# Kernel tuning notes

Hardware: AMD Instinct MI355X
Metric: run time of the kernel (lower is better)

## Reference

```python
import jax, jax.numpy as jnp
import numpy as np

N, E, D_IN, H, OUT = 50000, 800000, 128, 256, 2
BN_EPS = 1e-5
LN_EPS = 1e-5


def _xavier(k, fi, fo):
    lim = float(np.sqrt(6.0 / (fi + fo)))
    return jax.random.uniform(k, (fi, fo), minval=-lim, maxval=lim, dtype=jnp.float32)


def setup_inputs() -> dict:
    key = jax.random.key(0)
    ks = jax.random.split(key, 8)
    return {
        "x": jax.random.normal(ks[0], (N, D_IN), dtype=jnp.float32),
        "edge_index": jax.random.randint(ks[1], (2, E), 0, N, dtype=jnp.int32),
        "feature_scale": jnp.ones((D_IN,), jnp.float32),
        "feature_bias": jnp.zeros((D_IN,), jnp.float32),
        "bn0_g": jnp.ones((D_IN,), jnp.float32),
        "bn0_b": jnp.zeros((D_IN,), jnp.float32),
        "W1": _xavier(ks[2], D_IN, H), "b1": jnp.zeros((H,), jnp.float32),
        "bn1_g": jnp.ones((H,), jnp.float32), "bn1_b": jnp.zeros((H,), jnp.float32),
        "ln1_g": jnp.ones((H,), jnp.float32), "ln1_b": jnp.zeros((H,), jnp.float32),
        "W2": _xavier(ks[3], H, H), "b2": jnp.zeros((H,), jnp.float32),
        "bn2_g": jnp.ones((H,), jnp.float32), "bn2_b": jnp.zeros((H,), jnp.float32),
        "ln2_g": jnp.ones((H,), jnp.float32), "ln2_b": jnp.zeros((H,), jnp.float32),
        "Wout": _xavier(ks[4], H, OUT), "bout": jnp.zeros((OUT,), jnp.float32),
    }


def _batchnorm(x, g, b):
    # training-mode BatchNorm1d: batch stats over node axis, biased variance
    mu = jnp.mean(x, axis=0)
    var = jnp.mean(jnp.square(x - mu), axis=0)
    return g * (x - mu) * jax.lax.rsqrt(var + BN_EPS) + b


def _layernorm(x, g, b):
    mu = jnp.mean(x, axis=-1, keepdims=True)
    var = jnp.mean(jnp.square(x - mu), axis=-1, keepdims=True)
    return g * (x - mu) * jax.lax.rsqrt(var + LN_EPS) + b


def _gcn(x, W, b, src, dst, dinv):
    # PyG GCNConv with self-loops: D^{-1/2}(A+I)D^{-1/2} X W + b
    h = x @ W                                   # [N, F]
    norm = (dinv[src] * dinv[dst])[:, None]     # [E, 1]
    msg = h[src] * norm                         # [E, F] (dominant traffic)
    agg = jax.ops.segment_sum(msg, dst, num_segments=N)
    return agg + (dinv * dinv)[:, None] * h + b


def _forward(x, feature_scale, feature_bias, bn0_g, bn0_b,
             W1, b1, bn1_g, bn1_b, ln1_g, ln1_b,
             W2, b2, bn2_g, bn2_b, ln2_g, ln2_b,
             Wout, bout, edge_index):
    src, dst = edge_index[0], edge_index[1]
    deg = jax.ops.segment_sum(jnp.ones((E,), x.dtype), dst, num_segments=N) + 1.0
    dinv = jax.lax.rsqrt(deg)

    h = x * feature_scale + feature_bias
    h = _batchnorm(h, bn0_g, bn0_b)            # input_bn; dropout = identity (eval)

    # layer 0 (no residual: i == 0)
    h1 = _gcn(h, W1, b1, src, dst, dinv)
    h1 = jax.nn.relu(h1)
    h1 = _batchnorm(h1, bn1_g, bn1_b)
    h1 = _layernorm(h1, ln1_g, ln1_b)

    # layer 1 (residual add, shapes match)
    h2 = _gcn(h1, W2, b2, src, dst, dinv)
    h2 = jax.nn.relu(h2)
    h2 = _batchnorm(h2, bn2_g, bn2_b)
    h2 = _layernorm(h2, ln2_g, ln2_b)
    h2 = h2 + h1

    return h2 @ Wout + bout


def reference(x, edge_index, feature_scale, feature_bias, bn0_g, bn0_b,
              W1, b1, bn1_g, bn1_b, ln1_g, ln1_b,
              W2, b2, bn2_g, bn2_b, ln2_g, ln2_b,
              Wout, bout):
    return _forward(x, feature_scale, feature_bias, bn0_g, bn0_b,
                    W1, b1, bn1_g, bn1_b, ln1_g, ln1_b,
                    W2, b2, bn2_g, bn2_b, ln2_g, ln2_b,
                    Wout, bout, edge_index)
```

## Files before the change

kernel.cpp:

```cpp
#include <hip/hip_runtime.h>
#include <hip/hip_bf16.h>
#include <stdint.h>

#define N_NODES 50000
#define N_EDGES 800000
#define D_IN    128
#define H_DIM   256
#define BN_EPS  1e-5f
#define LN_EPS  1e-5f
#define NBLK2 1563
#define SLICE_ELEMS ((size_t)N_NODES * 32)
#define EDGE_CHUNK 3072
#define BN0_BLOCKS 256
#define PREPX_BLOCKS 6250
#define TR_BLOCKS 256
#define NBKT 196
#define CHUNK 4096
#define RCHUNKS 196

typedef float v4f __attribute__((ext_vector_type(4)));
typedef short v8s __attribute__((ext_vector_type(8)));

__device__ __forceinline__ float bflo(unsigned u){ return __uint_as_float(u << 16); }
__device__ __forceinline__ float bfhi(unsigned u){ return __uint_as_float(u & 0xffff0000u); }
__device__ __forceinline__ unsigned short f2bf(float f){
  unsigned u = __float_as_uint(f);
  u += 0x7fffu + ((u >> 16) & 1u);
  return (unsigned short)(u >> 16);
}
__device__ __forceinline__ unsigned pack2(float a, float b){
  return (unsigned)f2bf(a) | ((unsigned)f2bf(b) << 16);
}
__device__ __forceinline__ float wred(float v){
  #pragma unroll
  for (int m = 1; m < 64; m <<= 1) v += __shfl_xor(v, m, 64);
  return v;
}

__device__ __forceinline__ int block_excl_scan(int v){
  int t = threadIdx.x;
  int lane = t & 63, w = t >> 6;
  int inc = v;
  #pragma unroll
  for (int m = 1; m < 64; m <<= 1){
    int o = __shfl_up(inc, m, 64);
    if (lane >= m) inc += o;
  }
  __shared__ int wsum[4];
  if (lane == 63) wsum[w] = inc;
  __syncthreads();
  int base = 0;
  #pragma unroll
  for (int j = 0; j < 4; ++j) if (j < w) base += wsum[j];
  return base + inc - v;
}

__global__ __launch_bounds__(256) void bn0r1_k(const int* ei, const float* x,
                                               const float* fs, const float* fb,
                                               float* S, float* Q, int* ghist){
  int b = blockIdx.x, t = threadIdx.x;
  if (b >= BN0_BLOCKS){
    __shared__ int lh[NBKT];
    int b2 = b - BN0_BLOCKS;
    for (int i = t; i < NBKT; i += 256) lh[i] = 0;
    __syncthreads();
    int e0 = b2 * CHUNK;
    int n = min(CHUNK, N_EDGES - e0);
    for (int i = t; i < n; i += 256)
      atomicAdd(&lh[ei[N_EDGES + e0 + i] >> 8], 1);
    __syncthreads();
    if (t < NBKT && lh[t] > 0) atomicAdd(&ghist[t], lh[t]);
    return;
  }
  int cl = t & 31, rg = t >> 5;
  int c = cl * 4;
  float4 fs4 = *(const float4*)(fs + c);
  float4 fb4 = *(const float4*)(fb + c);
  float s0=0,s1=0,s2=0,s3=0,q0=0,q1=0,q2=0,q3=0;
  for (int row = b * 8 + rg; row < N_NODES; row += BN0_BLOCKS * 8){
    float4 xv = *(const float4*)(x + (size_t)row * D_IN + c);
    float v0 = xv.x * fs4.x + fb4.x;
    float v1 = xv.y * fs4.y + fb4.y;
    float v2 = xv.z * fs4.z + fb4.z;
    float v3 = xv.w * fs4.w + fb4.w;
    s0 += v0; s1 += v1; s2 += v2; s3 += v3;
    q0 += v0*v0; q1 += v1*v1; q2 += v2*v2; q3 += v3*v3;
  }
  __shared__ float red[256][8];
  red[t][0]=s0; red[t][1]=s1; red[t][2]=s2; red[t][3]=s3;
  red[t][4]=q0; red[t][5]=q1; red[t][6]=q2; red[t][7]=q3;
  __syncthreads();
  float* Sr = S + (b & 3) * D_IN;
  float* Qr = Q + (b & 3) * D_IN;
  if (t < 32){
    float a[8];
    #pragma unroll
    for (int i = 0; i < 8; ++i) a[i] = red[t][i];
    for (int j = 1; j < 8; ++j)
      #pragma unroll
      for (int i = 0; i < 8; ++i) a[i] += red[t + 32*j][i];
    #pragma unroll
    for (int i = 0; i < 4; ++i){ atomicAdd(&Sr[t*4+i], a[i]); atomicAdd(&Qr[t*4+i], a[4+i]); }
  }
}

__global__ __launch_bounds__(256) void scanb_k(const int* ghist, int* gcursor, int* bbase){
  int t = threadIdx.x;
  int v = (t < NBKT) ? ghist[t] : 0;
  int e = block_excl_scan(v);
  if (t < NBKT){ gcursor[t] = e; bbase[t] = e; }
  if (t == 0) bbase[NBKT] = N_EDGES;
}

__global__ __launch_bounds__(256) void r3_k(const int* ei, int* gcursor, unsigned* ebuf){
  __shared__ unsigned short dstS[CHUNK];
  __shared__ int lh[NBKT], cb[NBKT];
  int t = threadIdx.x;
  int e0 = blockIdx.x * CHUNK;
  int n = min(CHUNK, N_EDGES - e0);
  for (int i = t; i < NBKT; i += 256) lh[i] = 0;
  __syncthreads();
  for (int i = t; i < n; i += 256){
    int d = ei[N_EDGES + e0 + i];
    dstS[i] = (unsigned short)d;
    atomicAdd(&lh[d >> 8], 1);
  }
  __syncthreads();
  if (t < NBKT && lh[t] > 0) cb[t] = atomicAdd(&gcursor[t], lh[t]);
  __syncthreads();
  if (t < NBKT) lh[t] = 0;
  __syncthreads();
  for (int i = t; i < n; i += 256){
    int d = dstS[i];
    int bkt = d >> 8;
    int r = atomicAdd(&lh[bkt], 1);
    unsigned src = (unsigned)ei[e0 + i];
    ebuf[cb[bkt] + r] = ((unsigned)(d & 255) << 16) | src;
  }
}

__global__ __launch_bounds__(256) void r4a_k(const unsigned* ebuf, const int* bbase,
                                             int* cnt, int* dhist){
  __shared__ int h[256], dh[128];
  int t = threadIdx.x, b = blockIdx.x;
  h[t] = 0;
  if (t < 128) dh[t] = 0;
  __syncthreads();
  int lo = bbase[b], hi = bbase[b + 1];
  for (int i = lo + t; i < hi; i += 256)
    atomicAdd(&h[(ebuf[i] >> 16) & 255], 1);
  __syncthreads();
  int node = b * 256 + t;
  if (node < N_NODES){
    cnt[node] = h[t];
    atomicAdd(&dh[min(h[t], 127)], 1);
  }
  __syncthreads();
  if (t < 128 && dh[t] > 0) atomicAdd(&dhist[t], dh[t]);
}

__global__ __launch_bounds__(256) void dperm2_k(const int* cnt, const int* dhist, int* reserve,
                                                int* perm, int* rank, int* offs, float* dinv){
  __shared__ int ep_s[128], W_s[128], lb[128], lh[128], lc[128];
  int t = threadIdx.x;
  int v = (t < 128) ? dhist[t] : 0;
  int e1 = block_excl_scan(v);
  __syncthreads();
  int e2 = block_excl_scan((t < 128) ? v * t : 0);
  __syncthreads();
  if (t < 128){ ep_s[t] = e1; W_s[t] = e2; lh[t] = 0; lc[t] = 0; }
  __syncthreads();
  for (int i = blockIdx.x * 256 + t; i < N_NODES; i += 32 * 256)
    atomicAdd(&lh[min(cnt[i], 127)], 1);
  __syncthreads();
  if (t < 128 && lh[t] > 0) lb[t] = ep_s[t] + atomicAdd(&reserve[t], lh[t]);
  __syncthreads();
  for (int i = blockIdx.x * 256 + t; i < N_NODES; i += 32 * 256){
    int d = cnt[i];
    int b = min(d, 127);
    int r = atomicAdd(&lc[b], 1);
    int pos = lb[b] + r;
    perm[pos] = i;
    rank[i] = pos;
    offs[pos] = W_s[b] + (pos - ep_s[b]) * d;
    dinv[i] = rsqrtf((float)d + 1.0f);
  }
  if (blockIdx.x == 0 && t == 0) offs[N_NODES] = N_EDGES;
}

__global__ __launch_bounds__(256) void r4b_k(const unsigned* ebuf, const int* bbase,
                                             const int* rank, const int* offs,
                                             unsigned short* edges){
  __shared__ int curs[256];
  int t = threadIdx.x, b = blockIdx.x;
  int node = b * 256 + t;
  if (node < N_NODES) curs[t] = offs[rank[node]];
  __syncthreads();
  int lo = bbase[b], hi = bbase[b + 1];
  for (int i = lo + t; i < hi; i += 256){
    unsigned u = ebuf[i];
    int l8 = (u >> 16) & 255;
    int pos = atomicAdd(&curs[l8], 1);
    edges[pos] = (unsigned short)(u & 0xffffu);
  }
}

__global__ __launch_bounds__(256) void prep_k(const float* x, const float* S, const float* Q,
                                              const float* fs, const float* fb,
                                              const float* gg, const float* bb,
                                              unsigned short* xt,
                                              const float* W1, const float* W2,
                                              unsigned short* W1t, unsigned short* W2t){
  int b = blockIdx.x, t = threadIdx.x;
  if (b < PREPX_BLOCKS){
    int i = b * 256 + t;
    int row = i >> 5; int c = (i & 31) * 4;
    float4 Sv = *(const float4*)(S + c);
    float4 Qv = *(const float4*)(Q + c);
    #pragma unroll
    for (int rep = 1; rep < 4; ++rep){
      float4 s2 = *(const float4*)(S + rep * D_IN + c);
      float4 q2 = *(const float4*)(Q + rep * D_IN + c);
      Sv.x += s2.x; Sv.y += s2.y; Sv.z += s2.z; Sv.w += s2.w;
      Qv.x += q2.x; Qv.y += q2.y; Qv.z += q2.z; Qv.w += q2.w;
    }
    float4 fs4 = *(const float4*)(fs + c);
    float4 fb4 = *(const float4*)(fb + c);
    float4 gg4 = *(const float4*)(gg + c);
    float4 bb4 = *(const float4*)(bb + c);
    const float invN = 1.0f / N_NODES;
    float mu0 = Sv.x*invN, mu1 = Sv.y*invN, mu2 = Sv.z*invN, mu3 = Sv.w*invN;
    float r0 = rsqrtf(Qv.x*invN - mu0*mu0 + BN_EPS);
    float r1 = rsqrtf(Qv.y*invN - mu1*mu1 + BN_EPS);
    float r2 = rsqrtf(Qv.z*invN - mu2*mu2 + BN_EPS);
    float r3 = rsqrtf(Qv.w*invN - mu3*mu3 + BN_EPS);
    float a0 = gg4.x*r0*fs4.x, c0 = gg4.x*r0*(fb4.x - mu0) + bb4.x;
    float a1 = gg4.y*r1*fs4.y, c1 = gg4.y*r1*(fb4.y - mu1) + bb4.y;
    float a2 = gg4.z*r2*fs4.z, c2 = gg4.z*r2*(fb4.z - mu2) + bb4.z;
    float a3 = gg4.w*r3*fs4.w, c3 = gg4.w*r3*(fb4.w - mu3) + bb4.w;
    float4 xv = *(const float4*)(x + (size_t)row * D_IN + c);
    uint2 o;
    o.x = pack2(a0 * xv.x + c0, a1 * xv.y + c1);
    o.y = pack2(a2 * xv.z + c2, a3 * xv.w + c3);
    *(uint2*)(xt + (size_t)row * D_IN + c) = o;
    return;
  }
  int i = (b - PREPX_BLOCKS) * 256 + t;
  if (i < D_IN * H_DIM){
    int r = i / H_DIM, c = i % H_DIM;
    W1t[c * D_IN + r] = f2bf(W1[i]);
  }
  if (i < H_DIM * H_DIM){
    int r = i / H_DIM, c = i % H_DIM;
    W2t[c * H_DIM + r] = f2bf(W2[i]);
  }
}

template<int K>
__global__ __launch_bounds__(256) void gemm_k(const unsigned short* A, const unsigned short* Bt,
                                              const float* dinv, unsigned short* C, int M){
  __shared__ __align__(16) short smem[16896];
  __shared__ float dvs[64];
  short* As = smem;
  short* Bs = smem + 64 * 40;
  int t = threadIdx.x;
  int m0 = blockIdx.x * 64;
  int lane = t & 63;
  int w = t >> 6;
  int fr = lane & 15, quad = lane >> 4;
  if (t < 64) dvs[t] = (m0 + t < M) ? dinv[m0 + t] : 0.0f;
  v4f acc[4][4] = {};
  int sr = t >> 2;
  int sk = (t & 3) << 3;
  for (int k0 = 0; k0 < K; k0 += 32){
    __syncthreads();
    uint4 av = {0,0,0,0};
    int arow = m0 + sr;
    if (arow < M) av = *(const uint4*)(A + (size_t)arow * K + k0 + sk);
    *(uint4*)(&As[sr * 40 + sk]) = av;
    #pragma unroll
    for (int j = 0; j < 4; ++j){
      int brow = sr + 64 * j;
      uint4 bv = *(const uint4*)(Bt + (size_t)brow * K + k0 + sk);
      *(uint4*)(&Bs[brow * 40 + sk]) = bv;
    }
    __syncthreads();
    v8s af[4], bf[4];
    #pragma unroll
    for (int mi = 0; mi < 4; ++mi)
      af[mi] = *(const v8s*)(&As[(mi * 16 + fr) * 40 + quad * 8]);
    #pragma unroll
    for (int ni = 0; ni < 4; ++ni)
      bf[ni] = *(const v8s*)(&Bs[(w * 64 + ni * 16 + fr) * 40 + quad * 8]);
    #pragma unroll
    for (int mi = 0; mi < 4; ++mi)
      #pragma unroll
      for (int ni = 0; ni < 4; ++ni)
        acc[mi][ni] = __builtin_amdgcn_mfma_f32_16x16x32_bf16(af[mi], bf[ni], acc[mi][ni], 0, 0, 0);
  }
  __syncthreads();
  short* Cs = smem;
  #pragma unroll
  for (int mi = 0; mi < 4; ++mi)
    #pragma unroll
    for (int ni = 0; ni < 4; ++ni)
      #pragma unroll
      for (int r = 0; r < 4; ++r){
        int row = mi * 16 + quad * 4 + r;
        int col = w * 64 + ni * 16 + fr;
        Cs[row * 264 + col] = (short)f2bf(acc[mi][ni][r] * dvs[row]);
      }
  __syncthreads();
  int orow = t >> 2;
  int grow = m0 + orow;
  if (grow < M){
    #pragma unroll
    for (int j = 0; j < 4; ++j){
      int oc = (t & 3) * 16 + 64 * j;
      v8s v0 = *(const v8s*)(&Cs[orow * 264 + oc]);
      v8s v1 = *(const v8s*)(&Cs[orow * 264 + oc + 8]);
      *(v8s*)(&C[(size_t)(oc >> 5) * SLICE_ELEMS + (size_t)grow * 32 + (oc & 31)]) = v0;
      int oc1 = oc + 8;
      *(v8s*)(&C[(size_t)(oc1 >> 5) * SLICE_ELEMS + (size_t)grow * 32 + (oc1 & 31)]) = v1;
    }
  }
}

__global__ __launch_bounds__(256) void agg_k(const unsigned short* hs, const int* offsets,
                                             const unsigned short* edges, const int* perm,
                                             const float* dinv, const float* bias,
                                             unsigned short* g, float* pS, float* pQ){
  __shared__ unsigned eds32[EDGE_CHUNK / 2];
  __shared__ float wps[4][8][8];
  int t = threadIdx.x;
  int lane = t & 63;
  int wv = t >> 6;
  int slice = blockIdx.x & 7;
  int l8 = lane & 7;
  int nb = (blockIdx.x >> 3) * 32;
  int idx = nb + (t >> 3);
  int lastn = min(nb + 32, N_NODES);
  int blk0 = offsets[nb];
  int base = blk0 & ~1;
  int blkN = offsets[lastn];
  const unsigned* gsrc = (const unsigned*)(edges + base);
  int nu = min((blkN - base + 1) >> 1, EDGE_CHUNK / 2);
  for (int i = t; i < nu; i += 256)
    eds32[i] = gsrc[i];
  __syncthreads();
  bool act = idx < N_NODES;
  int node = act ? perm[idx] : 0;
  const unsigned short* hb = hs + (size_t)slice * SLICE_ELEMS;
  float4 bb = *(const float4*)(bias + slice * 32 + l8 * 4);
  uint2 sv = *(const uint2*)(hb + (size_t)node * 32 + l8 * 4);
  float a0 = bflo(sv.x), a1 = bfhi(sv.x);
  float a2 = bflo(sv.y), a3 = bfhi(sv.y);
  int e  = act ? offsets[idx] : 0;
  int e1 = act ? offsets[idx + 1] : 0;
  if ((e & 1) && e < e1){
    int ru = (e - base) >> 1;
    unsigned d = (ru < EDGE_CHUNK / 2) ? eds32[ru] : gsrc[ru];
    unsigned s = d >> 16;
    uint2 v = *(const uint2*)(hb + (size_t)s * 32 + l8 * 4);
    a0 += bflo(v.x); a1 += bfhi(v.x);
    a2 += bflo(v.y); a3 += bfhi(v.y);
    ++e;
  }
  for (; e + 16 <= e1; e += 16){
    int ru = (e - base) >> 1;
    unsigned dd[8];
    if (ru + 8 <= EDGE_CHUNK / 2){
      #pragma unroll
      for (int j = 0; j < 8; ++j) dd[j] = eds32[ru + j];
    } else {
      #pragma unroll
      for (int j = 0; j < 8; ++j) dd[j] = gsrc[ru + j];
    }
    uint2 v[16];
    #pragma unroll
    for (int j = 0; j < 8; ++j){
      v[2*j]   = *(const uint2*)(hb + (size_t)(dd[j] & 0xffffu) * 32 + l8 * 4);
      v[2*j+1] = *(const uint2*)(hb + (size_t)(dd[j] >> 16)     * 32 + l8 * 4);
    }
    #pragma unroll
    for (int j = 0; j < 16; ++j){
      a0 += bflo(v[j].x); a1 += bfhi(v[j].x);
      a2 += bflo(v[j].y); a3 += bfhi(v[j].y);
    }
  }
  if (e + 8 <= e1){
    int ru = (e - base) >> 1;
    unsigned dd[4];
    if (ru + 4 <= EDGE_CHUNK / 2){
      #pragma unroll
      for (int j = 0; j < 4; ++j) dd[j] = eds32[ru + j];
    } else {
      #pragma unroll
      for (int j = 0; j < 4; ++j) dd[j] = gsrc[ru + j];
    }
    uint2 v[8];
    #pragma unroll
    for (int j = 0; j < 4; ++j){
      v[2*j]   = *(const uint2*)(hb + (size_t)(dd[j] & 0xffffu) * 32 + l8 * 4);
      v[2*j+1] = *(const uint2*)(hb + (size_t)(dd[j] >> 16)     * 32 + l8 * 4);
    }
    #pragma unroll
    for (int j = 0; j < 8; ++j){
      a0 += bflo(v[j].x); a1 += bfhi(v[j].x);
      a2 += bflo(v[j].y); a3 += bfhi(v[j].y);
    }
    e += 8;
  }
  for (; e < e1; ++e){
    int r = e - base;
    unsigned d = ((r >> 1) < EDGE_CHUNK / 2) ? eds32[r >> 1] : gsrc[r >> 1];
    unsigned s = (r & 1) ? (d >> 16) : (d & 0xffffu);
    uint2 v = *(const uint2*)(hb + (size_t)s * 32 + l8 * 4);
    a0 += bflo(v.x); a1 += bfhi(v.x);
    a2 += bflo(v.y); a3 += bfhi(v.y);
  }
  float dv = dinv[node];
  float y0 = act ? fmaxf(dv * a0 + bb.x, 0.f) : 0.f;
  float y1 = act ? fmaxf(dv * a1 + bb.y, 0.f) : 0.f;
  float y2 = act ? fmaxf(dv * a2 + bb.z, 0.f) : 0.f;
  float y3 = act ? fmaxf(dv * a3 + bb.w, 0.f) : 0.f;
  if (act){
    uint2 o;
    o.x = pack2(y0, y1); o.y = pack2(y2, y3);
    *(uint2*)(g + (size_t)node * H_DIM + slice * 32 + l8 * 4) = o;
  }
  float q0 = y0*y0, q1 = y1*y1, q2 = y2*y2, q3 = y3*y3;
  #pragma unroll
  for (int m = 8; m < 64; m <<= 1){
    y0 += __shfl_xor(y0, m, 64); y1 += __shfl_xor(y1, m, 64);
    y2 += __shfl_xor(y2, m, 64); y3 += __shfl_xor(y3, m, 64);
    q0 += __shfl_xor(q0, m, 64); q1 += __shfl_xor(q1, m, 64);
    q2 += __shfl_xor(q2, m, 64); q3 += __shfl_xor(q3, m, 64);
  }
  if (lane < 8){
    wps[wv][l8][0] = y0; wps[wv][l8][1] = y1; wps[wv][l8][2] = y2; wps[wv][l8][3] = y3;
    wps[wv][l8][4] = q0; wps[wv][l8][5] = q1; wps[wv][l8][6] = q2; wps[wv][l8][7] = q3;
  }
  __syncthreads();
  if (t < 64){
    int tl8 = t >> 3, ti = t & 7;
    float v = wps[0][tl8][ti] + wps[1][tl8][ti] + wps[2][tl8][ti] + wps[3][tl8][ti];
    int col32 = tl8 * 4 + (ti & 3);
    if (ti < 4) pS[(size_t)blockIdx.x * 32 + col32] = v;
    else        pQ[(size_t)blockIdx.x * 32 + col32] = v;
  }
}

__global__ __launch_bounds__(1024) void redu_k(const float* pS, const float* pQ,
                                               const float* gg, const float* bb,
                                               float* sc, float* sh){
  __shared__ float ls[32][32], lq[32][32];
  int t = threadIdx.x;
  int slice = blockIdx.x;
  int grp = t >> 5, c32 = t & 31;
  float as = 0.f, aq = 0.f;
  for (int blk2 = grp; blk2 < NBLK2; blk2 += 32){
    size_t o = ((size_t)blk2 * 8 + slice) * 32 + c32;
    as += pS[o]; aq += pQ[o];
  }
  ls[grp][c32] = as; lq[grp][c32] = aq;
  __syncthreads();
  if (t < 32){
    float S = 0.f, Q = 0.f;
    #pragma unroll
    for (int gI = 0; gI < 32; ++gI){ S += ls[gI][t]; Q += lq[gI][t]; }
    int col = slice * 32 + t;
    const float invN = 1.0f / N_NODES;
    float mu = S * invN;
    float rs = rsqrtf(Q * invN - mu * mu + BN_EPS);
    float s = gg[col] * rs;
    sc[col] = s;
    sh[col] = bb[col] - s * mu;
  }
}

__global__ __launch_bounds__(256) void apply1_k(const unsigned short* g, const float* sc, const float* sh,
                                                const float* lng, const float* lnb, unsigned short* h1){
  int lane = threadIdx.x & 63;
  int row = blockIdx.x * 4 + (threadIdx.x >> 6);
  if (row >= N_NODES) return;
  int c = lane * 4;
  float4 s4 = *(const float4*)(sc + c);
  float4 h4 = *(const float4*)(sh + c);
  uint2 u = *(const uint2*)(g + (size_t)row * H_DIM + c);
  float v0 = s4.x * bflo(u.x) + h4.x;
  float v1 = s4.y * bfhi(u.x) + h4.y;
  float v2 = s4.z * bflo(u.y) + h4.z;
  float v3 = s4.w * bfhi(u.y) + h4.w;
  float sum = wred(v0 + v1 + v2 + v3);
  float sq  = wred(v0*v0 + v1*v1 + v2*v2 + v3*v3);
  float mu = sum * (1.0f / H_DIM);
  float var = sq * (1.0f / H_DIM) - mu * mu;
  float rs = rsqrtf(var + LN_EPS);
  float4 g4 = *(const float4*)(lng + c);
  float4 b4 = *(const float4*)(lnb + c);
  float y0 = g4.x * (v0 - mu) * rs + b4.x;
  float y1 = g4.y * (v1 - mu) * rs + b4.y;
  float y2 = g4.z * (v2 - mu) * rs + b4.z;
  float y3 = g4.w * (v3 - mu) * rs + b4.w;
  uint2 o; o.x = pack2(y0, y1); o.y = pack2(y2, y3);
  *(uint2*)(h1 + (size_t)row * H_DIM + c) = o;
}

__global__ __launch_bounds__(256) void apply2_k(const unsigned short* g, const float* sc, const float* sh,
                                                const float* lng, const float* lnb,
                                                const unsigned short* h1, const float* Wout,
                                                const float* bout, float* out){
  int lane = threadIdx.x & 63;
  int row = blockIdx.x * 4 + (threadIdx.x >> 6);
  if (row >= N_NODES) return;
  int c = lane * 4;
  float4 s4 = *(const float4*)(sc + c);
  float4 h4 = *(const float4*)(sh + c);
  uint2 u = *(const uint2*)(g + (size_t)row * H_DIM + c);
  float v0 = s4.x * bflo(u.x) + h4.x;
  float v1 = s4.y * bfhi(u.x) + h4.y;
  float v2 = s4.z * bflo(u.y) + h4.z;
  float v3 = s4.w * bfhi(u.y) + h4.w;
  float sum = wred(v0 + v1 + v2 + v3);
  float sq  = wred(v0*v0 + v1*v1 + v2*v2 + v3*v3);
  float mu = sum * (1.0f / H_DIM);
  float var = sq * (1.0f / H_DIM) - mu * mu;
  float rs = rsqrtf(var + LN_EPS);
  float4 g4 = *(const float4*)(lng + c);
  float4 b4 = *(const float4*)(lnb + c);
  uint2 hr = *(const uint2*)(h1 + (size_t)row * H_DIM + c);
  float y0 = g4.x * (v0 - mu) * rs + b4.x + bflo(hr.x);
  float y1 = g4.y * (v1 - mu) * rs + b4.y + bfhi(hr.x);
  float y2 = g4.z * (v2 - mu) * rs + b4.z + bflo(hr.y);
  float y3 = g4.w * (v3 - mu) * rs + b4.w + bfhi(hr.y);
  float4 w0 = *(const float4*)(Wout + c * 2);
  float4 w1 = *(const float4*)(Wout + c * 2 + 4);
  float o0 = y0 * w0.x + y1 * w0.z + y2 * w1.x + y3 * w1.z;
  float o1 = y0 * w0.y + y1 * w0.w + y2 * w1.y + y3 * w1.w;
  o0 = wred(o0); o1 = wred(o1);
  if (lane == 0){
    out[(size_t)row * 2 + 0] = o0 + bout[0];
    out[(size_t)row * 2 + 1] = o1 + bout[1];
  }
}

extern "C" void kernel_launch(void* const* d_in, const int* in_sizes, int n_in,
                              void* d_out, int out_size, void* d_ws, size_t ws_size,
                              hipStream_t stream) {
  const float* x    = (const float*)d_in[0];
  const int*   ei   = (const int*)d_in[1];
  const float* fs   = (const float*)d_in[2];
  const float* fb   = (const float*)d_in[3];
  const float* bn0g = (const float*)d_in[4];
  const float* bn0b = (const float*)d_in[5];
  const float* W1   = (const float*)d_in[6];
  const float* b1   = (const float*)d_in[7];
  const float* bn1g = (const float*)d_in[8];
  const float* bn1b = (const float*)d_in[9];
  const float* ln1g = (const float*)d_in[10];
  const float* ln1b = (const float*)d_in[11];
  const float* W2   = (const float*)d_in[12];
  const float* b2   = (const float*)d_in[13];
  const float* bn2g = (const float*)d_in[14];
  const float* bn2b = (const float*)d_in[15];
  const float* ln2g = (const float*)d_in[16];
  const float* ln2b = (const float*)d_in[17];
  const float* Wout = (const float*)d_in[18];
  const float* bout = (const float*)d_in[19];
  float* out = (float*)d_out;

  char* w = (char*)d_ws;
  float* bn0S  = (float*)(w + 0);
  float* bn0Q  = (float*)(w + 2048);
  int*   dhist = (int*)(w + 4096);
  int*   reserve = (int*)(w + 4608);
  int*   ghist  = (int*)(w + 5120);
  int*   gcursor= (int*)(w + 5904);
  const size_t ZERO_BYTES = 6688;
  int*   bbase  = (int*)(w + 6688);
  float* sc1   = (float*)(w + 7488);
  float* sh1   = (float*)(w + 8512);
  float* sc2   = (float*)(w + 9536);
  float* sh2   = (float*)(w + 10560);
  int*   cnt   = (int*)(w + 11584);
  float* dinv  = (float*)(w + 211584);
  int*   offs  = (int*)(w + 411584);
  int*   perm  = (int*)(w + 611712);
  int*   rank  = (int*)(w + 811712);
  unsigned short* edges = (unsigned short*)(w + 1011712);
  unsigned short* xt   = (unsigned short*)(w + 2611712);
  unsigned short* W1t  = (unsigned short*)(w + 15411712);
  unsigned short* W2t  = (unsigned short*)(w + 15477248);
  unsigned short* hlin = (unsigned short*)(w + 15608320);
  unsigned*       ebuf = (unsigned*)(w + 15608320);
  unsigned short* gbuf = (unsigned short*)(w + 41208320);
  unsigned short* h1   = (unsigned short*)(w + 66808320);
  float* pS    = (float*)(w + 92408320);
  float* pQ    = (float*)(w + 94008832);

  (void)in_sizes; (void)n_in; (void)out_size; (void)ws_size;

  hipMemsetAsync(d_ws, 0, ZERO_BYTES, stream);

  bn0r1_k<<<BN0_BLOCKS + RCHUNKS, 256, 0, stream>>>(ei, x, fs, fb, bn0S, bn0Q, ghist);
  scanb_k<<<1, 256, 0, stream>>>(ghist, gcursor, bbase);
  r3_k<<<RCHUNKS, 256, 0, stream>>>(ei, gcursor, ebuf);
  r4a_k<<<NBKT, 256, 0, stream>>>(ebuf, bbase, cnt, dhist);
  dperm2_k<<<32, 256, 0, stream>>>(cnt, dhist, reserve, perm, rank, offs, dinv);
  r4b_k<<<NBKT, 256, 0, stream>>>(ebuf, bbase, rank, offs, edges);
  prep_k<<<PREPX_BLOCKS + TR_BLOCKS, 256, 0, stream>>>(x, bn0S, bn0Q, fs, fb, bn0g, bn0b,
                                                       xt, W1, W2, W1t, W2t);

  int ggrid = (N_NODES + 63) / 64;
  int agg_blocks = NBLK2 * 8;

  gemm_k<D_IN><<<ggrid, 256, 0, stream>>>(xt, W1t, dinv, hlin, N_NODES);
  agg_k<<<agg_blocks, 256, 0, stream>>>(hlin, offs, edges, perm, dinv, b1, gbuf, pS, pQ);
  redu_k<<<8, 1024, 0, stream>>>(pS, pQ, bn1g, bn1b, sc1, sh1);
  apply1_k<<<(N_NODES + 3) / 4, 256, 0, stream>>>(gbuf, sc1, sh1, ln1g, ln1b, h1);

  gemm_k<H_DIM><<<ggrid, 256, 0, stream>>>(h1, W2t, dinv, hlin, N_NODES);
  agg_k<<<agg_blocks, 256, 0, stream>>>(hlin, offs, edges, perm, dinv, b2, gbuf, pS, pQ);
  redu_k<<<8, 1024, 0, stream>>>(pS, pQ, bn2g, bn2b, sc2, sh2);
  apply2_k<<<(N_NODES + 3) / 4, 256, 0, stream>>>(gbuf, sc2, sh2, ln2g, ln2b, h1, Wout, bout, out);
}
```

Baseline: 371.0 us.

## Widen aggregation gathers to 16B, fold scan kernels, fuse r4b with prep

The aggregation kernel now uses 4 lanes per node, each doing a 16-byte gather of 8 bf16 features, instead of 8 lanes doing 8-byte gathers. Each block covers 64 nodes, so the grid is halved, and the unroll drops from 16 edges to 8. The separate bucket-scan kernel is removed: r3, r4a and the merged r4b/prep kernel each recompute the exclusive scan from the histogram, and r4b is fused into prep to cut two launches. The LayerNorm apply kernels now use 32 lanes per row with 16-byte loads. Risks are fewer gathers in flight per node from the smaller unroll and a redundant scan in every block.

```diff
diff --git a/kernel.cpp b/kernel.cpp
--- a/kernel.cpp
+++ b/kernel.cpp
@@ -8,7 +8,7 @@
 #define H_DIM   256
 #define BN_EPS  1e-5f
 #define LN_EPS  1e-5f
-#define NBLK2 1563
+#define NBLK2 782
 #define SLICE_ELEMS ((size_t)N_NODES * 32)
 #define EDGE_CHUNK 3072
 #define BN0_BLOCKS 256
@@ -30,11 +30,6 @@
 }
 __device__ __forceinline__ unsigned pack2(float a, float b){
   return (unsigned)f2bf(a) | ((unsigned)f2bf(b) << 16);
-}
-__device__ __forceinline__ float wred(float v){
-  #pragma unroll
-  for (int m = 1; m < 64; m <<= 1) v += __shfl_xor(v, m, 64);
-  return v;
 }
 
 __device__ __forceinline__ int block_excl_scan(int v){
@@ -104,29 +99,23 @@
   }
 }
 
-__global__ __launch_bounds__(256) void scanb_k(const int* ghist, int* gcursor, int* bbase){
+__global__ __launch_bounds__(256) void r3_k(const int* ei, const int* ghist, int* gcursor, unsigned* ebuf){
+  __shared__ unsigned short dstS[CHUNK];
+  __shared__ int lh[NBKT], cb[NBKT], sbb[NBKT];
   int t = threadIdx.x;
   int v = (t < NBKT) ? ghist[t] : 0;
-  int e = block_excl_scan(v);
-  if (t < NBKT){ gcursor[t] = e; bbase[t] = e; }
-  if (t == 0) bbase[NBKT] = N_EDGES;
-}
-
-__global__ __launch_bounds__(256) void r3_k(const int* ei, int* gcursor, unsigned* ebuf){
-  __shared__ unsigned short dstS[CHUNK];
-  __shared__ int lh[NBKT], cb[NBKT];
-  int t = threadIdx.x;
+  int epre = block_excl_scan(v);
+  if (t < NBKT){ sbb[t] = epre; lh[t] = 0; }
+  __syncthreads();
   int e0 = blockIdx.x * CHUNK;
   int n = min(CHUNK, N_EDGES - e0);
-  for (int i = t; i < NBKT; i += 256) lh[i] = 0;
-  __syncthreads();
   for (int i = t; i < n; i += 256){
     int d = ei[N_EDGES + e0 + i];
     dstS[i] = (unsigned short)d;
     atomicAdd(&lh[d >> 8], 1);
   }
   __syncthreads();
-  if (t < NBKT && lh[t] > 0) cb[t] = atomicAdd(&gcursor[t], lh[t]);
+  if (t < NBKT && lh[t] > 0) cb[t] = sbb[t] + atomicAdd(&gcursor[t], lh[t]);
   __syncthreads();
   if (t < NBKT) lh[t] = 0;
   __syncthreads();
@@ -139,14 +128,18 @@
   }
 }
 
-__global__ __launch_bounds__(256) void r4a_k(const unsigned* ebuf, const int* bbase,
+__global__ __launch_bounds__(256) void r4a_k(const unsigned* ebuf, const int* ghist,
                                              int* cnt, int* dhist){
-  __shared__ int h[256], dh[128];
+  __shared__ int h[256], dh[128], sbb[NBKT + 1];
   int t = threadIdx.x, b = blockIdx.x;
+  int v = (t < NBKT) ? ghist[t] : 0;
+  int epre = block_excl_scan(v);
+  if (t < NBKT) sbb[t] = epre;
+  if (t == NBKT - 1) sbb[NBKT] = epre + v;
   h[t] = 0;
   if (t < 128) dh[t] = 0;
   __syncthreads();
-  int lo = bbase[b], hi = bbase[b + 1];
+  int lo = sbb[b], hi = sbb[b + 1];
   for (int i = lo + t; i < hi; i += 256)
     atomicAdd(&h[(ebuf[i] >> 16) & 255], 1);
   __syncthreads();
@@ -188,32 +181,36 @@
   if (blockIdx.x == 0 && t == 0) offs[N_NODES] = N_EDGES;
 }
 
-__global__ __launch_bounds__(256) void r4b_k(const unsigned* ebuf, const int* bbase,
-                                             const int* rank, const int* offs,
-                                             unsigned short* edges){
-  __shared__ int curs[256];
-  int t = threadIdx.x, b = blockIdx.x;
-  int node = b * 256 + t;
-  if (node < N_NODES) curs[t] = offs[rank[node]];
-  __syncthreads();
-  int lo = bbase[b], hi = bbase[b + 1];
-  for (int i = lo + t; i < hi; i += 256){
-    unsigned u = ebuf[i];
-    int l8 = (u >> 16) & 255;
-    int pos = atomicAdd(&curs[l8], 1);
-    edges[pos] = (unsigned short)(u & 0xffffu);
-  }
-}
-
-__global__ __launch_bounds__(256) void prep_k(const float* x, const float* S, const float* Q,
-                                              const float* fs, const float* fb,
-                                              const float* gg, const float* bb,
-                                              unsigned short* xt,
-                                              const float* W1, const float* W2,
-                                              unsigned short* W1t, unsigned short* W2t){
+__global__ __launch_bounds__(256) void r4bprep_k(const unsigned* ebuf, const int* ghist,
+                                                 const int* rank, const int* offs,
+                                                 unsigned short* edges,
+                                                 const float* x, const float* S, const float* Q,
+                                                 const float* fs, const float* fb,
+                                                 const float* gg, const float* bb,
+                                                 unsigned short* xt,
+                                                 const float* W1, const float* W2,
+                                                 unsigned short* W1t, unsigned short* W2t){
+  __shared__ int curs[256], sbb[NBKT + 1];
   int b = blockIdx.x, t = threadIdx.x;
-  if (b < PREPX_BLOCKS){
-    int i = b * 256 + t;
+  if (b < NBKT){
+    int v = (t < NBKT) ? ghist[t] : 0;
+    int epre = block_excl_scan(v);
+    if (t < NBKT) sbb[t] = epre;
+    if (t == NBKT - 1) sbb[NBKT] = epre + v;
+    int node = b * 256 + t;
+    if (node < N_NODES) curs[t] = offs[rank[node]];
+    __syncthreads();
+    int lo = sbb[b], hi = sbb[b + 1];
+    for (int i = lo + t; i < hi; i += 256){
+      unsigned u = ebuf[i];
+      int l8 = (u >> 16) & 255;
+      int pos = atomicAdd(&curs[l8], 1);
+      edges[pos] = (unsigned short)(u & 0xffffu);
+    }
+    return;
+  }
+  if (b < NBKT + PREPX_BLOCKS){
+    int i = (b - NBKT) * 256 + t;
     int row = i >> 5; int c = (i & 31) * 4;
     float4 Sv = *(const float4*)(S + c);
     float4 Qv = *(const float4*)(Q + c);
@@ -245,7 +242,7 @@
     *(uint2*)(xt + (size_t)row * D_IN + c) = o;
     return;
   }
-  int i = (b - PREPX_BLOCKS) * 256 + t;
+  int i = (b - NBKT - PREPX_BLOCKS) * 256 + t;
   if (i < D_IN * H_DIM){
     int r = i / H_DIM, c = i % H_DIM;
     W1t[c * D_IN + r] = f2bf(W1[i]);
@@ -326,20 +323,23 @@
   }
 }
 
+#define ACC8(vv) { a0 += bflo(vv.x); a1 += bfhi(vv.x); a2 += bflo(vv.y); a3 += bfhi(vv.y); \
+                   a4 += bflo(vv.z); a5 += bfhi(vv.z); a6 += bflo(vv.w); a7 += bfhi(vv.w); }
+
 __global__ __launch_bounds__(256) void agg_k(const unsigned short* hs, const int* offsets,
                                              const unsigned short* edges, const int* perm,
                                              const float* dinv, const float* bias,
                                              unsigned short* g, float* pS, float* pQ){
   __shared__ unsigned eds32[EDGE_CHUNK / 2];
-  __shared__ float wps[4][8][8];
+  __shared__ float wps[4][4][16];
   int t = threadIdx.x;
   int lane = t & 63;
   int wv = t >> 6;
   int slice = blockIdx.x & 7;
-  int l8 = lane & 7;
-  int nb = (blockIdx.x >> 3) * 32;
-  int idx = nb + (t >> 3);
-  int lastn = min(nb + 32, N_NODES);
+  int l4 = lane & 3;
+  int nb = (blockIdx.x >> 3) * 64;
+  int idx = nb + (t >> 2);
+  int lastn = min(nb + 64, N_NODES);
   int blk0 = offsets[nb];
   int base = blk0 & ~1;
   int blkN = offsets[lastn];
@@ -350,45 +350,24 @@
   __syncthreads();
   bool act = idx < N_NODES;
   int node = act ? perm[idx] : 0;
-  const unsigned short* hb = hs + (size_t)slice * SLICE_ELEMS;
-  float4 bb = *(const float4*)(bias + slice * 32 + l8 * 4);
-  uint2 sv = *(const uint2*)(hb + (size_t)node * 32 + l8 * 4);
+  const uint4* hb4 = (const uint4*)(hs + (size_t)slice * SLICE_ELEMS);
+  float4 bb0 = *(const float4*)(bias + slice * 32 + l4 * 8);
+  float4 bb1 = *(const float4*)(bias + slice * 32 + l4 * 8 + 4);
+  uint4 sv = hb4[(size_t)node * 4 + l4];
   float a0 = bflo(sv.x), a1 = bfhi(sv.x);
   float a2 = bflo(sv.y), a3 = bfhi(sv.y);
+  float a4 = bflo(sv.z), a5 = bfhi(sv.z);
+  float a6 = bflo(sv.w), a7 = bfhi(sv.w);
   int e  = act ? offsets[idx] : 0;
   int e1 = act ? offsets[idx + 1] : 0;
   if ((e & 1) && e < e1){
     int ru = (e - base) >> 1;
     unsigned d = (ru < EDGE_CHUNK / 2) ? eds32[ru] : gsrc[ru];
-    unsigned s = d >> 16;
-    uint2 v = *(const uint2*)(hb + (size_t)s * 32 + l8 * 4);
-    a0 += bflo(v.x); a1 += bfhi(v.x);
-    a2 += bflo(v.y); a3 += bfhi(v.y);
+    uint4 vv = hb4[(size_t)(d >> 16) * 4 + l4];
+    ACC8(vv);
     ++e;
   }
-  for (; e + 16 <= e1; e += 16){
-    int ru = (e - base) >> 1;
-    unsigned dd[8];
-    if (ru + 8 <= EDGE_CHUNK / 2){
-      #pragma unroll
-      for (int j = 0; j < 8; ++j) dd[j] = eds32[ru + j];
-    } else {
-      #pragma unroll
-      for (int j = 0; j < 8; ++j) dd[j] = gsrc[ru + j];
-    }
-    uint2 v[16];
-    #pragma unroll
-    for (int j = 0; j < 8; ++j){
-      v[2*j]   = *(const uint2*)(hb + (size_t)(dd[j] & 0xffffu) * 32 + l8 * 4);
-      v[2*j+1] = *(const uint2*)(hb + (size_t)(dd[j] >> 16)     * 32 + l8 * 4);
-    }
-    #pragma unroll
-    for (int j = 0; j < 16; ++j){
-      a0 += bflo(v[j].x); a1 += bfhi(v[j].x);
-      a2 += bflo(v[j].y); a3 += bfhi(v[j].y);
-    }
-  }
-  if (e + 8 <= e1){
+  for (; e + 8 <= e1; e += 8){
     int ru = (e - base) >> 1;
     unsigned dd[4];
     if (ru + 4 <= EDGE_CHUNK / 2){
@@ -398,55 +377,80 @@
       #pragma unroll
       for (int j = 0; j < 4; ++j) dd[j] = gsrc[ru + j];
     }
-    uint2 v[8];
+    uint4 v[8];
     #pragma unroll
     for (int j = 0; j < 4; ++j){
-      v[2*j]   = *(const uint2*)(hb + (size_t)(dd[j] & 0xffffu) * 32 + l8 * 4);
-      v[2*j+1] = *(const uint2*)(hb + (size_t)(dd[j] >> 16)     * 32 + l8 * 4);
-    }
-    #pragma unroll
-    for (int j = 0; j < 8; ++j){
-      a0 += bflo(v[j].x); a1 += bfhi(v[j].x);
-      a2 += bflo(v[j].y); a3 += bfhi(v[j].y);
-    }
-    e += 8;
+      v[2*j]   = hb4[(size_t)(dd[j] & 0xffffu) * 4 + l4];
+      v[2*j+1] = hb4[(size_t)(dd[j] >> 16)     * 4 + l4];
+    }
+    #pragma unroll
+    for (int j = 0; j < 8; ++j) ACC8(v[j]);
+  }
+  if (e + 4 <= e1){
+    int ru = (e - base) >> 1;
+    unsigned dd[2];
+    if (ru + 2 <= EDGE_CHUNK / 2){
+      dd[0] = eds32[ru]; dd[1] = eds32[ru + 1];
+    } else {
+      dd[0] = gsrc[ru]; dd[1] = gsrc[ru + 1];
+    }
+    uint4 v[4];
+    #pragma unroll
+    for (int j = 0; j < 2; ++j){
+      v[2*j]   = hb4[(size_t)(dd[j] & 0xffffu) * 4 + l4];
+      v[2*j+1] = hb4[(size_t)(dd[j] >> 16)     * 4 + l4];
+    }
+    #pragma unroll
+    for (int j = 0; j < 4; ++j) ACC8(v[j]);
+    e += 4;
   }
   for (; e < e1; ++e){
     int r = e - base;
     unsigned d = ((r >> 1) < EDGE_CHUNK / 2) ? eds32[r >> 1] : gsrc[r >> 1];
     unsigned s = (r & 1) ? (d >> 16) : (d & 0xffffu);
-    uint2 v = *(const uint2*)(hb + (size_t)s * 32 + l8 * 4);
-    a0 += bflo(v.x); a1 += bfhi(v.x);
-    a2 += bflo(v.y); a3 += bfhi(v.y);
+    uint4 vv = hb4[(size_t)s * 4 + l4];
+    ACC8(vv);
   }
   float dv = dinv[node];
-  float y0 = act ? fmaxf(dv * a0 + bb.x, 0.f) : 0.f;
-  float y1 = act ? fmaxf(dv * a1 + bb.y, 0.f) : 0.f;
-  float y2 = act ? fmaxf(dv * a2 + bb.z, 0.f) : 0.f;
-  float y3 = act ? fmaxf(dv * a3 + bb.w, 0.f) : 0.f;
+  float y0 = act ? fmaxf(dv * a0 + bb0.x, 0.f) : 0.f;
+  float y1 = act ? fmaxf(dv * a1 + bb0.y, 0.f) : 0.f;
+  float y2 = act ? fmaxf(dv * a2 + bb0.z, 0.f) : 0.f;
+  float y3 = act ? fmaxf(dv * a3 + bb0.w, 0.f) : 0.f;
+  float y4 = act ? fmaxf(dv * a4 + bb1.x, 0.f) : 0.f;
+  float y5 = act ? fmaxf(dv * a5 + bb1.y, 0.f) : 0.f;
+  float y6 = act ? fmaxf(dv * a6 + bb1.z, 0.f) : 0.f;
+  float y7 = act ? fmaxf(dv * a7 + bb1.w, 0.f) : 0.f;
   if (act){
-    uint2 o;
+    uint4 o;
     o.x = pack2(y0, y1); o.y = pack2(y2, y3);
-    *(uint2*)(g + (size_t)node * H_DIM + slice * 32 + l8 * 4) = o;
+    o.z = pack2(y4, y5); o.w = pack2(y6, y7);
+    *(uint4*)(g + (size_t)node * H_DIM + slice * 32 + l4 * 8) = o;
   }
   float q0 = y0*y0, q1 = y1*y1, q2 = y2*y2, q3 = y3*y3;
+  float q4 = y4*y4, q5 = y5*y5, q6 = y6*y6, q7 = y7*y7;
   #pragma unroll
-  for (int m = 8; m < 64; m <<= 1){
+  for (int m = 4; m < 64; m <<= 1){
     y0 += __shfl_xor(y0, m, 64); y1 += __shfl_xor(y1, m, 64);
     y2 += __shfl_xor(y2, m, 64); y3 += __shfl_xor(y3, m, 64);
+    y4 += __shfl_xor(y4, m, 64); y5 += __shfl_xor(y5, m, 64);
+    y6 += __shfl_xor(y6, m, 64); y7 += __shfl_xor(y7, m, 64);
     q0 += __shfl_xor(q0, m, 64); q1 += __shfl_xor(q1, m, 64);
     q2 += __shfl_xor(q2, m, 64); q3 += __shfl_xor(q3, m, 64);
-  }
-  if (lane < 8){
-    wps[wv][l8][0] = y0; wps[wv][l8][1] = y1; wps[wv][l8][2] = y2; wps[wv][l8][3] = y3;
-    wps[wv][l8][4] = q0; wps[wv][l8][5] = q1; wps[wv][l8][6] = q2; wps[wv][l8][7] = q3;
+    q4 += __shfl_xor(q4, m, 64); q5 += __shfl_xor(q5, m, 64);
+    q6 += __shfl_xor(q6, m, 64); q7 += __shfl_xor(q7, m, 64);
+  }
+  if (lane < 4){
+    wps[wv][lane][0] = y0; wps[wv][lane][1] = y1; wps[wv][lane][2] = y2; wps[wv][lane][3] = y3;
+    wps[wv][lane][4] = y4; wps[wv][lane][5] = y5; wps[wv][lane][6] = y6; wps[wv][lane][7] = y7;
+    wps[wv][lane][8] = q0; wps[wv][lane][9] = q1; wps[wv][lane][10] = q2; wps[wv][lane][11] = q3;
+    wps[wv][lane][12] = q4; wps[wv][lane][13] = q5; wps[wv][lane][14] = q6; wps[wv][lane][15] = q7;
   }
   __syncthreads();
   if (t < 64){
-    int tl8 = t >> 3, ti = t & 7;
-    float v = wps[0][tl8][ti] + wps[1][tl8][ti] + wps[2][tl8][ti] + wps[3][tl8][ti];
-    int col32 = tl8 * 4 + (ti & 3);
-    if (ti < 4) pS[(size_t)blockIdx.x * 32 + col32] = v;
+    int tl = t >> 4, ti = t & 15;
+    float v = wps[0][tl][ti] + wps[1][tl][ti] + wps[2][tl][ti] + wps[3][tl][ti];
+    int col32 = tl * 8 + (ti & 7);
+    if (ti < 8) pS[(size_t)blockIdx.x * 32 + col32] = v;
     else        pQ[(size_t)blockIdx.x * 32 + col32] = v;
   }
 }
@@ -481,65 +485,94 @@
 
 __global__ __launch_bounds__(256) void apply1_k(const unsigned short* g, const float* sc, const float* sh,
                                                 const float* lng, const float* lnb, unsigned short* h1){
-  int lane = threadIdx.x & 63;
-  int row = blockIdx.x * 4 + (threadIdx.x >> 6);
+  int t = threadIdx.x;
+  int lane32 = t & 31;
+  int row = blockIdx.x * 8 + (t >> 5);
   if (row >= N_NODES) return;
-  int c = lane * 4;
-  float4 s4 = *(const float4*)(sc + c);
-  float4 h4 = *(const float4*)(sh + c);
-  uint2 u = *(const uint2*)(g + (size_t)row * H_DIM + c);
-  float v0 = s4.x * bflo(u.x) + h4.x;
-  float v1 = s4.y * bfhi(u.x) + h4.y;
-  float v2 = s4.z * bflo(u.y) + h4.z;
-  float v3 = s4.w * bfhi(u.y) + h4.w;
-  float sum = wred(v0 + v1 + v2 + v3);
-  float sq  = wred(v0*v0 + v1*v1 + v2*v2 + v3*v3);
+  int c = lane32 * 8;
+  float4 s40 = *(const float4*)(sc + c);
+  float4 s41 = *(const float4*)(sc + c + 4);
+  float4 h40 = *(const float4*)(sh + c);
+  float4 h41 = *(const float4*)(sh + c + 4);
+  uint4 u = *(const uint4*)(g + (size_t)row * H_DIM + c);
+  float v0 = s40.x * bflo(u.x) + h40.x;
+  float v1 = s40.y * bfhi(u.x) + h40.y;
+  float v2 = s40.z * bflo(u.y) + h40.z;
+  float v3 = s40.w * bfhi(u.y) + h40.w;
+  float v4 = s41.x * bflo(u.z) + h41.x;
+  float v5 = s41.y * bfhi(u.z) + h41.y;
+  float v6 = s41.z * bflo(u.w) + h41.z;
+  float v7 = s41.w * bfhi(u.w) + h41.w;
+  float sum = v0+v1+v2+v3+v4+v5+v6+v7;
+  float sq  = v0*v0+v1*v1+v2*v2+v3*v3+v4*v4+v5*v5+v6*v6+v7*v7;
+  #pragma unroll
+  for (int m = 1; m < 32; m <<= 1){ sum += __shfl_xor(sum, m, 64); sq += __shfl_xor(sq, m, 64); }
   float mu = sum * (1.0f / H_DIM);
   float var = sq * (1.0f / H_DIM) - mu * mu;
   float rs = rsqrtf(var + LN_EPS);
-  float4 g4 = *(const float4*)(lng + c);
-  float4 b4 = *(const float4*)(lnb + c);
-  float y0 = g4.x * (v0 - mu) * rs + b4.x;
-  float y1 = g4.y * (v1 - mu) * rs + b4.y;
-  float y2 = g4.z * (v2 - mu) * rs + b4.z;
-  float y3 = g4.w * (v3 - mu) * rs + b4.w;
-  uint2 o; o.x = pack2(y0, y1); o.y = pack2(y2, y3);
-  *(uint2*)(h1 + (size_t)row * H_DIM + c) = o;
+  float4 g40 = *(const float4*)(lng + c);
+  float4 g41 = *(const float4*)(lng + c + 4);
+  float4 b40 = *(const float4*)(lnb + c);
+  float4 b41 = *(const float4*)(lnb + c + 4);
+  uint4 o;
+  o.x = pack2(g40.x * (v0 - mu) * rs + b40.x, g40.y * (v1 - mu) * rs + b40.y);
+  o.y = pack2(g40.z * (v2 - mu) * rs + b40.z, g40.w * (v3 - mu) * rs + b40.w);
+  o.z = pack2(g41.x * (v4 - mu) * rs + b41.x, g41.y * (v5 - mu) * rs + b41.y);
+  o.w = pack2(g41.z * (v6 - mu) * rs + b41.z, g41.w * (v7 - mu) * rs + b41.w);
+  *(uint4*)(h1 + (size_t)row * H_DIM + c) = o;
 }
 
 __global__ __launch_bounds__(256) void apply2_k(const unsigned short* g, const float* sc, const float* sh,
                                                 const float* lng, const float* lnb,
                                                 const unsigned short* h1, const float* Wout,
                                                 const float* bout, float* out){
-  int lane = threadIdx.x & 63;
-  int row = blockIdx.x * 4 + (threadIdx.x >> 6);
+  int t = threadIdx.x;
+  int lane32 = t & 31;
+  int row = blockIdx.x * 8 + (t >> 5);
   if (row >= N_NODES) return;
-  int c = lane * 4;
-  float4 s4 = *(const float4*)(sc + c);
-  float4 h4 = *(const float4*)(sh + c);
-  uint2 u = *(const uint2*)(g + (size_t)row * H_DIM + c);
-  float v0 = s4.x * bflo(u.x) + h4.x;
-  float v1 = s4.y * bfhi(u.x) + h4.y;
-  float v2 = s4.z * bflo(u.y) + h4.z;
-  float v3 = s4.w * bfhi(u.y) + h4.w;
-  float sum = wred(v0 + v1 + v2 + v3);
-  float sq  = wred(v0*v0 + v1*v1 + v2*v2 + v3*v3);
+  int c = lane32 * 8;
+  float4 s40 = *(const float4*)(sc + c);
+  float4 s41 = *(const float4*)(sc + c + 4);
+  float4 h40 = *(const float4*)(sh + c);
+  float4 h41 = *(const float4*)(sh + c + 4);
+  uint4 u = *(const uint4*)(g + (size_t)row * H_DIM + c);
+  float v0 = s40.x * bflo(u.x) + h40.x;
+  float v1 = s40.y * bfhi(u.x) + h40.y;
+  float v2 = s40.z * bflo(u.y) + h40.z;
+  float v3 = s40.w * bfhi(u.y) + h40.w;
+  float v4 = s41.x * bflo(u.z) + h41.x;
+  float v5 = s41.y * bfhi(u.z) + h41.y;
+  float v6 = s41.z * bflo(u.w) + h41.z;
+  float v7 = s41.w * bfhi(u.w) + h41.w;
+  float sum = v0+v1+v2+v3+v4+v5+v6+v7;
+  float sq  = v0*v0+v1*v1+v2*v2+v3*v3+v4*v4+v5*v5+v6*v6+v7*v7;
+  #pragma unroll
+  for (int m = 1; m < 32; m <<= 1){ sum += __shfl_xor(sum, m, 64); sq += __shfl_xor(sq, m, 64); }
   float mu = sum * (1.0f / H_DIM);
   float var = sq * (1.0f / H_DIM) - mu * mu;
   float rs = rsqrtf(var + LN_EPS);
-  float4 g4 = *(const float4*)(lng + c);
-  float4 b4 = *(const float4*)(lnb + c);
-  uint2 hr = *(const uint2*)(h1 + (size_t)row * H_DIM + c);
-  float y0 = g4.x * (v0 - mu) * rs + b4.x + bflo(hr.x);
-  float y1 = g4.y * (v1 - mu) * rs + b4.y + bfhi(hr.x);
-  float y2 = g4.z * (v2 - mu) * rs + b4.z + bflo(hr.y);
-  float y3 = g4.w * (v3 - mu) * rs + b4.w + bfhi(hr.y);
+  float4 g40 = *(const float4*)(lng + c);
+  float4 g41 = *(const float4*)(lng + c + 4);
+  float4 b40 = *(const float4*)(lnb + c);
+  float4 b41 = *(const float4*)(lnb + c + 4);
+  uint4 hr = *(const uint4*)(h1 + (size_t)row * H_DIM + c);
+  float y0 = g40.x * (v0 - mu) * rs + b40.x + bflo(hr.x);
+  float y1 = g40.y * (v1 - mu) * rs + b40.y + bfhi(hr.x);
+  float y2 = g40.z * (v2 - mu) * rs + b40.z + bflo(hr.y);
+  float y3 = g40.w * (v3 - mu) * rs + b40.w + bfhi(hr.y);
+  float y4 = g41.x * (v4 - mu) * rs + b41.x + bflo(hr.z);
+  float y5 = g41.y * (v5 - mu) * rs + b41.y + bfhi(hr.z);
+  float y6 = g41.z * (v6 - mu) * rs + b41.z + bflo(hr.w);
+  float y7 = g41.w * (v7 - mu) * rs + b41.w + bfhi(hr.w);
   float4 w0 = *(const float4*)(Wout + c * 2);
   float4 w1 = *(const float4*)(Wout + c * 2 + 4);
-  float o0 = y0 * w0.x + y1 * w0.z + y2 * w1.x + y3 * w1.z;
-  float o1 = y0 * w0.y + y1 * w0.w + y2 * w1.y + y3 * w1.w;
-  o0 = wred(o0); o1 = wred(o1);
-  if (lane == 0){
+  float4 w2 = *(const float4*)(Wout + c * 2 + 8);
+  float4 w3 = *(const float4*)(Wout + c * 2 + 12);
+  float o0 = y0*w0.x + y1*w0.z + y2*w1.x + y3*w1.z + y4*w2.x + y5*w2.z + y6*w3.x + y7*w3.z;
+  float o1 = y0*w0.y + y1*w0.w + y2*w1.y + y3*w1.w + y4*w2.y + y5*w2.w + y6*w3.y + y7*w3.w;
+  #pragma unroll
+  for (int m = 1; m < 32; m <<= 1){ o0 += __shfl_xor(o0, m, 64); o1 += __shfl_xor(o1, m, 64); }
+  if (lane32 == 0){
     out[(size_t)row * 2 + 0] = o0 + bout[0];
     out[(size_t)row * 2 + 1] = o1 + bout[1];
   }
@@ -578,7 +611,6 @@
   int*   ghist  = (int*)(w + 5120);
   int*   gcursor= (int*)(w + 5904);
   const size_t ZERO_BYTES = 6688;
-  int*   bbase  = (int*)(w + 6688);
   float* sc1   = (float*)(w + 7488);
   float* sh1   = (float*)(w + 8512);
   float* sc2   = (float*)(w + 9536);
@@ -604,13 +636,11 @@
   hipMemsetAsync(d_ws, 0, ZERO_BYTES, stream);
 
   bn0r1_k<<<BN0_BLOCKS + RCHUNKS, 256, 0, stream>>>(ei, x, fs, fb, bn0S, bn0Q, ghist);
-  scanb_k<<<1, 256, 0, stream>>>(ghist, gcursor, bbase);
-  r3_k<<<RCHUNKS, 256, 0, stream>>>(ei, gcursor, ebuf);
-  r4a_k<<<NBKT, 256, 0, stream>>>(ebuf, bbase, cnt, dhist);
+  r3_k<<<RCHUNKS, 256, 0, stream>>>(ei, ghist, gcursor, ebuf);
+  r4a_k<<<NBKT, 256, 0, stream>>>(ebuf, ghist, cnt, dhist);
   dperm2_k<<<32, 256, 0, stream>>>(cnt, dhist, reserve, perm, rank, offs, dinv);
-  r4b_k<<<NBKT, 256, 0, stream>>>(ebuf, bbase, rank, offs, edges);
-  prep_k<<<PREPX_BLOCKS + TR_BLOCKS, 256, 0, stream>>>(x, bn0S, bn0Q, fs, fb, bn0g, bn0b,
-                                                       xt, W1, W2, W1t, W2t);
+  r4bprep_k<<<NBKT + PREPX_BLOCKS + TR_BLOCKS, 256, 0, stream>>>(
+      ebuf, ghist, rank, offs, edges, x, bn0S, bn0Q, fs, fb, bn0g, bn0b, xt, W1, W2, W1t, W2t);
 
   int ggrid = (N_NODES + 63) / 64;
   int agg_blocks = NBLK2 * 8;
@@ -618,10 +648,10 @@
   gemm_k<D_IN><<<ggrid, 256, 0, stream>>>(xt, W1t, dinv, hlin, N_NODES);
   agg_k<<<agg_blocks, 256, 0, stream>>>(hlin, offs, edges, perm, dinv, b1, gbuf, pS, pQ);
   redu_k<<<8, 1024, 0, stream>>>(pS, pQ, bn1g, bn1b, sc1, sh1);
-  apply1_k<<<(N_NODES + 3) / 4, 256, 0, stream>>>(gbuf, sc1, sh1, ln1g, ln1b, h1);
+  apply1_k<<<(N_NODES + 7) / 8, 256, 0, stream>>>(gbuf, sc1, sh1, ln1g, ln1b, h1);
 
   gemm_k<H_DIM><<<ggrid, 256, 0, stream>>>(h1, W2t, dinv, hlin, N_NODES);
   agg_k<<<agg_blocks, 256, 0, stream>>>(hlin, offs, edges, perm, dinv, b2, gbuf, pS, pQ);
   redu_k<<<8, 1024, 0, stream>>>(pS, pQ, bn2g, bn2b, sc2, sh2);
-  apply2_k<<<(N_NODES + 3) / 4, 256, 0, stream>>>(gbuf, sc2, sh2, ln2g, ln2b, h1, Wout, bout, out);
-}
+  apply2_k<<<(N_NODES + 7) / 8, 256, 0, stream>>>(gbuf, sc2, sh2, ln2g, ln2b, h1, Wout, bout, out);
+}
```

New measurement: 340.5 us. 1.09x faster.
